# Performance work log

Measured on AMD Instinct MI355X. Metric: run time of the kernel, lower is better.

## Reference

```python
import jax, jax.numpy as jnp
import numpy as np

N_NODES = 50000
N_EDGES = 1600000
IN_FEATS = 512
N_HIDDEN = 128
N_CLASSES = 40


def setup_inputs() -> dict:
    key = jax.random.key(0)
    k1, k2, k3, k4, k5, k6, k7 = jax.random.split(key, 7)
    features = jax.random.normal(k1, (N_NODES, IN_FEATS), dtype=jnp.float32)
    src = jax.random.randint(k2, (N_EDGES,), 0, N_NODES)
    dst = jax.random.randint(k3, (N_EDGES,), 0, N_NODES)
    # Glorot-ish init for weights, zeros for biases (DGL GraphConv defaults)
    W1 = jax.random.normal(k4, (IN_FEATS, N_HIDDEN), dtype=jnp.float32) / np.sqrt(IN_FEATS)
    b1 = jnp.zeros((N_HIDDEN,), dtype=jnp.float32)
    W2 = jax.random.normal(k5, (N_HIDDEN, N_CLASSES), dtype=jnp.float32) / np.sqrt(N_HIDDEN)
    b2 = jnp.zeros((N_CLASSES,), dtype=jnp.float32)
    return {"features": features, "W1": W1, "b1": b1, "W2": W2, "b2": b2,
            "src": src, "dst": dst}


def _norms(src, dst, n_nodes):
    ones = jnp.ones(src.shape[0], dtype=jnp.float32)
    deg_out = jax.ops.segment_sum(ones, src, num_segments=n_nodes)
    deg_in = jax.ops.segment_sum(ones, dst, num_segments=n_nodes)
    # clamp degree >= 1 as DGL does
    norm_src = jax.lax.rsqrt(jnp.maximum(deg_out, 1.0))
    norm_dst = jax.lax.rsqrt(jnp.maximum(deg_in, 1.0))
    return norm_src, norm_dst


def _graph_conv(x, W, b, src, dst, norm_src, norm_dst, n_nodes):
    # DGL GraphConv with norm='both'; in_feats > out_feats so W applied first
    h = x @ W                                   # [N, out]
    h = h * norm_src[:, None]                   # src-side D^{-1/2}
    msgs = h[src]                               # gather [E, out]
    agg = jax.ops.segment_sum(msgs, dst, num_segments=n_nodes)  # scatter-add
    agg = agg * norm_dst[:, None]               # dst-side D^{-1/2}
    return agg + b


def reference(features, W1, b1, W2, b2, src, dst):
    norm_src, norm_dst = _norms(src, dst, N_NODES)
    h = _graph_conv(features, W1, b1, src, dst, norm_src, norm_dst, N_NODES)
    h = jax.nn.relu(h)
    # dropout is identity at inference
    h = _graph_conv(h, W2, b2, src, dst, norm_src, norm_dst, N_NODES)
    return h
```

## Files before the change

kernel.cpp:

```cpp
#include <hip/hip_runtime.h>
#include <hip/hip_bf16.h>

#define N_NODES 50000
#define N_EDGES 1600000
#define IN_FEATS 512
#define N_HIDDEN 128
#define N_CLASSES 40
#define NBKT 782
#define NBLK 800
#define EPB 2000
#define NROWPAD 50048

typedef __attribute__((ext_vector_type(8))) short bf16x8;
typedef __attribute__((ext_vector_type(4))) float f32x4;

__device__ __forceinline__ unsigned short f2bf(float f) {
    unsigned u = __float_as_uint(f);
    u = (u + 0x7FFFu + ((u >> 16) & 1u)) >> 16;
    return (unsigned short)u;
}
__device__ __forceinline__ float bf2f(unsigned short h) {
    return __uint_as_float(((unsigned)h) << 16);
}
__device__ __forceinline__ unsigned pk_bf(float a, float b) {
    __hip_bfloat162 h = __float22bfloat162_rn(make_float2(a, b));
    union { __hip_bfloat162 v; unsigned u; } c;
    c.v = h;
    return c.u;
}

__device__ __forceinline__ void cvt8(float4 a, float4 b, bf16x8& h, bf16x8& l) {
    unsigned h0 = pk_bf(a.x, a.y), h1 = pk_bf(a.z, a.w);
    unsigned h2 = pk_bf(b.x, b.y), h3 = pk_bf(b.z, b.w);
    unsigned l0 = pk_bf(a.x - __uint_as_float(h0 << 16),
                        a.y - __uint_as_float(h0 & 0xffff0000u));
    unsigned l1 = pk_bf(a.z - __uint_as_float(h1 << 16),
                        a.w - __uint_as_float(h1 & 0xffff0000u));
    unsigned l2 = pk_bf(b.x - __uint_as_float(h2 << 16),
                        b.y - __uint_as_float(h2 & 0xffff0000u));
    unsigned l3 = pk_bf(b.z - __uint_as_float(h3 << 16),
                        b.w - __uint_as_float(h3 & 0xffff0000u));
    union U { unsigned u[4]; bf16x8 v; };
    U H; H.u[0] = h0; H.u[1] = h1; H.u[2] = h2; H.u[3] = h3; h = H.v;
    U L; L.u[0] = l0; L.u[1] = l1; L.u[2] = l2; L.u[3] = l3; l = L.v;
}

__device__ __forceinline__ int imin(int a, int b) { return a < b ? a : b; }

__global__ __launch_bounds__(256) void setup_cvt(
    const float* __restrict__ W1, const float* __restrict__ W2,
    unsigned short* __restrict__ W1ch, unsigned short* __restrict__ W1cl,
    unsigned short* __restrict__ W2th, unsigned short* __restrict__ W2tl) {
    int i = blockIdx.x * 256 + threadIdx.x;
    if (i < IN_FEATS * N_HIDDEN) {
        int k = i >> 7, c = i & 127;
        float v = W1[i];
        unsigned short h = f2bf(v);
        int o = (k >> 5) * 4096 + c * 32 + (k & 31);
        W1ch[o] = h;
        W1cl[o] = f2bf(v - bf2f(h));
    } else {
        int j = i - IN_FEATS * N_HIDDEN;
        int n = j >> 7, k = j & 127;
        float v = (n < N_CLASSES) ? W2[k * N_CLASSES + n] : 0.f;
        unsigned short h = f2bf(v);
        W2th[n * 128 + k] = h;
        W2tl[n * 128 + k] = f2bf(v - bf2f(h));
    }
}


#define MFJ(AH, AL, BH, BL, ACC)                                              \
    ACC = __builtin_amdgcn_mfma_f32_16x16x32_bf16(AH, BH, ACC, 0, 0, 0);      \
    ACC = __builtin_amdgcn_mfma_f32_16x16x32_bf16(AH, BL, ACC, 0, 0, 0);      \
    ACC = __builtin_amdgcn_mfma_f32_16x16x32_bf16(AL, BH, ACC, 0, 0, 0);

#define CHUNK_COMPUTE(FRAGBASE, KC)                                           \
    {                                                                         \
        const unsigned short* wk  = wbh + (KC) * 4096;                        \
        const unsigned short* wkl = wbl + (KC) * 4096;                        \
        bf16x8 bh0 = *(const bf16x8*)(wk);                                    \
        bf16x8 bh1 = *(const bf16x8*)(wk + 512);                              \
        bf16x8 bl0 = *(const bf16x8*)(wkl);                                   \
        bf16x8 bl1 = *(const bf16x8*)(wkl + 512);                             \
        const unsigned short* fb = (FRAGBASE);                                \
        bf16x8 ah0 = *(const bf16x8*)(fb + (0 * 64 + lane) * 8);              \
        bf16x8 ah1 = *(const bf16x8*)(fb + (1 * 64 + lane) * 8);              \
        bf16x8 ah2 = *(const bf16x8*)(fb + (2 * 64 + lane) * 8);              \
        bf16x8 ah3 = *(const bf16x8*)(fb + (3 * 64 + lane) * 8);              \
        bf16x8 al0 = *(const bf16x8*)(fb + 2048 + (0 * 64 + lane) * 8);       \
        bf16x8 al1 = *(const bf16x8*)(fb + 2048 + (1 * 64 + lane) * 8);       \
        bf16x8 al2 = *(const bf16x8*)(fb + 2048 + (2 * 64 + lane) * 8);       \
        bf16x8 al3 = *(const bf16x8*)(fb + 2048 + (3 * 64 + lane) * 8);       \
        MFJ(ah0, al0, bh0, bl0, acc[0][0]) MFJ(ah0, al0, bh1, bl1, acc[0][1]) \
        MFJ(ah1, al1, bh0, bl0, acc[1][0]) MFJ(ah1, al1, bh1, bl1, acc[1][1]) \
        MFJ(ah2, al2, bh0, bl0, acc[2][0]) MFJ(ah2, al2, bh1, bl1, acc[2][1]) \
        MFJ(ah3, al3, bh0, bl0, acc[3][0]) MFJ(ah3, al3, bh1, bl1, acc[3][1]) \
    }

__global__ __launch_bounds__(256) void megaA(
    const int* __restrict__ src, const int* __restrict__ dst,
    int* __restrict__ histD, int* __restrict__ histS,
    const float* __restrict__ X, const unsigned short* __restrict__ Wch,
    const unsigned short* __restrict__ Wcl, unsigned short* __restrict__ Hb) {
    __shared__ __align__(16) unsigned char smem[32768];
    const int tid = threadIdx.x;

    if (blockIdx.x >= NBKT) {
        int* hd = (int*)smem;
        int* hs = hd + NBKT;
        int b = blockIdx.x - NBKT;
        for (int i = tid; i < NBKT; i += 256) { hd[i] = 0; hs[i] = 0; }
        __syncthreads();
        int e0 = b * EPB;
        for (int i = tid; i < EPB; i += 256) {
            atomicAdd(&hd[dst[e0 + i] >> 6], 1);
            atomicAdd(&hs[src[e0 + i] >> 6], 1);
        }
        __syncthreads();
        for (int i = tid; i < NBKT; i += 256) {
            histD[b * NBKT + i] = hd[i];
            histS[b * NBKT + i] = hs[i];
        }
        return;
    }
    typedef unsigned short ush;
    ush* lds = (ush*)smem;

    const int lane = tid & 63;
    const int wv = tid >> 6;
    const int m = lane & 15;
    const int q = lane >> 4;
    const int q8 = q * 8;
    const int row0 = blockIdx.x * 64;

    const unsigned short* wbh = Wch + (wv * 32 + m) * 32 + q8;
    const unsigned short* wbl = Wcl + (wv * 32 + m) * 32 + q8;

    const int srow = (tid >> 6) * 16 + (tid & 15);
    const int sq8  = ((tid >> 4) & 3) * 8;
    const float* xp = &X[(size_t)imin(row0 + srow, N_NODES - 1) * IN_FEATS + sq8];

    f32x4 acc[4][2];
#pragma unroll
    for (int i = 0; i < 4; i++)
#pragma unroll
        for (int j = 0; j < 2; j++) acc[i][j] = (f32x4){0.f, 0.f, 0.f, 0.f};

    {
        float4 c00 = *(const float4*)(xp),      c01 = *(const float4*)(xp + 4);
        float4 c10 = *(const float4*)(xp + 32), c11 = *(const float4*)(xp + 36);
        bf16x8 h, l;
        cvt8(c00, c01, h, l);
        *(bf16x8*)(lds + tid * 8) = h;
        *(bf16x8*)(lds + 2048 + tid * 8) = l;
        cvt8(c10, c11, h, l);
        *(bf16x8*)(lds + 4096 + tid * 8) = h;
        *(bf16x8*)(lds + 6144 + tid * 8) = l;
    }
    float4 a00 = *(const float4*)(xp + 64), a01 = *(const float4*)(xp + 68);
    float4 a10 = *(const float4*)(xp + 96), a11 = *(const float4*)(xp + 100);
    __syncthreads();

    for (int pp = 0; pp < 8; pp++) {
        if (pp < 7) {
            ush* bs = lds + ((pp + 1) & 1) * 8192;
            bf16x8 h, l;
            cvt8(a00, a01, h, l);
            *(bf16x8*)(bs + tid * 8) = h;
            *(bf16x8*)(bs + 2048 + tid * 8) = l;
            cvt8(a10, a11, h, l);
            *(bf16x8*)(bs + 4096 + tid * 8) = h;
            *(bf16x8*)(bs + 6144 + tid * 8) = l;
        }
        if (pp < 6) {
            const float* xq = xp + (pp + 2) * 64;
            a00 = *(const float4*)(xq);      a01 = *(const float4*)(xq + 4);
            a10 = *(const float4*)(xq + 32); a11 = *(const float4*)(xq + 36);
        }
        const ush* br = lds + (pp & 1) * 8192;
        CHUNK_COMPUTE(br,        2 * pp)
        CHUNK_COMPUTE(br + 4096, 2 * pp + 1)
        if (pp < 7) __syncthreads();
    }

#pragma unroll
    for (int i = 0; i < 4; i++) {
#pragma unroll
        for (int r = 0; r < 4; r++) {
            int grow = row0 + i * 16 + q * 4 + r;
            if (grow < N_NODES) {
#pragma unroll
                for (int j = 0; j < 2; j++)
                    Hb[(size_t)grow * N_HIDDEN + wv * 32 + j * 16 + m] = f2bf(acc[i][j][r]);
            }
        }
    }
}

__global__ __launch_bounds__(256) void p2_local(
    const int* __restrict__ histD, const int* __restrict__ histS,
    int* __restrict__ baseD, int* __restrict__ baseS,
    int* __restrict__ totD, int* __restrict__ totS) {
    int wv = threadIdx.x >> 6, lane = threadIdx.x & 63;
    int w = blockIdx.x * 4 + wv;
    if (w >= NBKT) return;
    int runD = 0, runS = 0;
#pragma unroll
    for (int c = 0; c < 13; c++) {
        int blk = c * 64 + lane;
        int vD = 0, vS = 0;
        if (blk < NBLK) {
            vD = histD[blk * NBKT + w];
            vS = histS[blk * NBKT + w];
        }
        int iD = vD, iS = vS;
#pragma unroll
        for (int off = 1; off < 64; off <<= 1) {
            int tD = __shfl_up(iD, off);
            int tS = __shfl_up(iS, off);
            if (lane >= off) { iD += tD; iS += tS; }
        }
        if (blk < NBLK) {
            baseD[blk * NBKT + w] = runD + iD - vD;
            baseS[blk * NBKT + w] = runS + iS - vS;
        }
        runD += __shfl(iD, 63);
        runS += __shfl(iS, 63);
    }
    if (lane == 0) { totD[w] = runD; totS[w] = runS; }
}

__global__ __launch_bounds__(1024) void p2_small(
    const int* __restrict__ totD, const int* __restrict__ totS,
    int* __restrict__ bucket_base, int* __restrict__ srcb_base,
    int* __restrict__ offsets) {
    __shared__ int part[1024];
    int t = threadIdx.x;
    int v = (t < NBKT) ? totD[t] : 0;
    part[t] = v;
    __syncthreads();
    for (int off = 1; off < 1024; off <<= 1) {
        int x = (t >= off) ? part[t - off] : 0;
        __syncthreads();
        part[t] += x;
        __syncthreads();
    }
    if (t < NBKT) bucket_base[t] = part[t] - v;
    if (t == 0) { bucket_base[NBKT] = N_EDGES; offsets[N_NODES] = N_EDGES; }
    __syncthreads();
    v = (t < NBKT) ? totS[t] : 0;
    part[t] = v;
    __syncthreads();
    for (int off = 1; off < 1024; off <<= 1) {
        int x = (t >= off) ? part[t - off] : 0;
        __syncthreads();
        part[t] += x;
        __syncthreads();
    }
    if (t < NBKT) srcb_base[t] = part[t] - v;
    if (t == 0) srcb_base[NBKT] = N_EDGES;
}

__global__ __launch_bounds__(256) void p3_scatter(
    const int* __restrict__ src, const int* __restrict__ dst,
    const int* __restrict__ baseD, const int* __restrict__ baseS,
    const int* __restrict__ bucket_base, const int* __restrict__ srcb_base,
    unsigned int* __restrict__ edata, unsigned char* __restrict__ srcv) {
    __shared__ int curD[NBKT], curS[NBKT];
    int t = threadIdx.x, b = blockIdx.x;
    for (int i = t; i < NBKT; i += 256) {
        curD[i] = bucket_base[i] + baseD[b * NBKT + i];
        curS[i] = srcb_base[i] + baseS[b * NBKT + i];
    }
    __syncthreads();
    int e0 = b * EPB;
    for (int i = t; i < EPB; i += 256) {
        int s = src[e0 + i], d = dst[e0 + i];
        int slotD = atomicAdd(&curD[d >> 6], 1);
        edata[slotD] = (unsigned)s | ((unsigned)(d & 63) << 16);
        int slotS = atomicAdd(&curS[s >> 6], 1);
        srcv[slotS] = (unsigned char)(s & 63);
    }
}

__global__ __launch_bounds__(256) void p4_fused(
    const int* __restrict__ srcb_base, const unsigned char* __restrict__ srcv,
    const int* __restrict__ bucket_base, const unsigned int* __restrict__ edata,
    int* __restrict__ offsets, float* __restrict__ norm_src,
    float* __restrict__ norm_dst, unsigned short* __restrict__ sorted_src) {
    __shared__ int cntS[64], cntD[64], cur[64];
    int t = threadIdx.x, b = blockIdx.x;
    if (t < 64) { cntS[t] = 0; cntD[t] = 0; }
    __syncthreads();
    int s0 = srcb_base[b], s1 = srcb_base[b + 1];
    for (int i = s0 + t; i < s1; i += 256) atomicAdd(&cntS[srcv[i]], 1);
    int d0 = bucket_base[b], d1 = bucket_base[b + 1];
    for (int i = d0 + t; i < d1; i += 256)
        atomicAdd(&cntD[(edata[i] >> 16) & 63], 1);
    __syncthreads();
    if (t == 0) {
        int run = 0;
        for (int i = 0; i < 64; i++) { cur[i] = run; run += cntD[i]; }
    }
    __syncthreads();
    if (t < 64) {
        int node = b * 64 + t;
        if (node < N_NODES) {
            norm_src[node] = rsqrtf(fmaxf((float)cntS[t], 1.0f));
            offsets[node] = d0 + cur[t];
            norm_dst[node] = rsqrtf(fmaxf((float)cntD[t], 1.0f));
        }
    }
    __syncthreads();
    for (int i = d0 + t; i < d1; i += 256) {
        unsigned e = edata[i];
        int slot = atomicAdd(&cur[(e >> 16) & 63], 1);
        sorted_src[d0 + slot] = (unsigned short)(e & 0xFFFFu);
    }
}

#define FMA8(W, NS)                                                   \
    acc0 = fmaf(__uint_as_float((W).x << 16), NS, acc0);              \
    acc1 = fmaf(__uint_as_float((W).x & 0xffff0000u), NS, acc1);      \
    acc2 = fmaf(__uint_as_float((W).y << 16), NS, acc2);              \
    acc3 = fmaf(__uint_as_float((W).y & 0xffff0000u), NS, acc3);      \
    acc4 = fmaf(__uint_as_float((W).z << 16), NS, acc4);              \
    acc5 = fmaf(__uint_as_float((W).z & 0xffff0000u), NS, acc5);      \
    acc6 = fmaf(__uint_as_float((W).w << 16), NS, acc6);              \
    acc7 = fmaf(__uint_as_float((W).w & 0xffff0000u), NS, acc7);

__global__ __launch_bounds__(256) void agg1_kernel(
    const int* __restrict__ offsets, const unsigned short* __restrict__ sorted_src,
    const unsigned short* __restrict__ Hb, const float* __restrict__ norm_dst,
    const float* __restrict__ norm_src, const float* __restrict__ b1,
    unsigned short* __restrict__ H1h, unsigned short* __restrict__ H1l) {
    int wid = (blockIdx.x * 256 + threadIdx.x) >> 6;
    int lane = threadIdx.x & 63;
    if (wid >= N_NODES) return;
    int start = offsets[wid], end = offsets[wid + 1];
    int quad = lane >> 4;
    int c8 = (lane & 15) * 8;
    float acc0 = 0.f, acc1 = 0.f, acc2 = 0.f, acc3 = 0.f;
    float acc4 = 0.f, acc5 = 0.f, acc6 = 0.f, acc7 = 0.f;
    int base = start;
    for (; base + 16 <= end; base += 16) {
        int e0 = sorted_src[base + quad];
        int e1 = sorted_src[base + 4 + quad];
        int e2 = sorted_src[base + 8 + quad];
        int e3 = sorted_src[base + 12 + quad];
        float n0 = norm_src[e0], n1 = norm_src[e1];
        float n2 = norm_src[e2], n3 = norm_src[e3];
        uint4 w0 = *(const uint4*)&Hb[(size_t)e0 * N_HIDDEN + c8];
        uint4 w1 = *(const uint4*)&Hb[(size_t)e1 * N_HIDDEN + c8];
        uint4 w2 = *(const uint4*)&Hb[(size_t)e2 * N_HIDDEN + c8];
        uint4 w3 = *(const uint4*)&Hb[(size_t)e3 * N_HIDDEN + c8];
        FMA8(w0, n0);
        FMA8(w1, n1);
        FMA8(w2, n2);
        FMA8(w3, n3);
    }
    for (; base + 4 <= end; base += 4) {
        int e = sorted_src[base + quad];
        float n = norm_src[e];
        uint4 w = *(const uint4*)&Hb[(size_t)e * N_HIDDEN + c8];
        FMA8(w, n);
    }
    int rem = end - base;
    if (quad < rem) {
        int e = sorted_src[base + quad];
        float n = norm_src[e];
        uint4 w = *(const uint4*)&Hb[(size_t)e * N_HIDDEN + c8];
        FMA8(w, n);
    }
    acc0 += __shfl_xor(acc0, 16); acc0 += __shfl_xor(acc0, 32);
    acc1 += __shfl_xor(acc1, 16); acc1 += __shfl_xor(acc1, 32);
    acc2 += __shfl_xor(acc2, 16); acc2 += __shfl_xor(acc2, 32);
    acc3 += __shfl_xor(acc3, 16); acc3 += __shfl_xor(acc3, 32);
    acc4 += __shfl_xor(acc4, 16); acc4 += __shfl_xor(acc4, 32);
    acc5 += __shfl_xor(acc5, 16); acc5 += __shfl_xor(acc5, 32);
    acc6 += __shfl_xor(acc6, 16); acc6 += __shfl_xor(acc6, 32);
    acc7 += __shfl_xor(acc7, 16); acc7 += __shfl_xor(acc7, 32);
    if (quad == 0) {
        float nd = norm_dst[wid];
        float ns = norm_src[wid];
        float4 ba = *(const float4*)&b1[c8];
        float4 bb = *(const float4*)&b1[c8 + 4];
        float o[8];
        o[0] = fmaxf(acc0 * nd + ba.x, 0.f) * ns;
        o[1] = fmaxf(acc1 * nd + ba.y, 0.f) * ns;
        o[2] = fmaxf(acc2 * nd + ba.z, 0.f) * ns;
        o[3] = fmaxf(acc3 * nd + ba.w, 0.f) * ns;
        o[4] = fmaxf(acc4 * nd + bb.x, 0.f) * ns;
        o[5] = fmaxf(acc5 * nd + bb.y, 0.f) * ns;
        o[6] = fmaxf(acc6 * nd + bb.z, 0.f) * ns;
        o[7] = fmaxf(acc7 * nd + bb.w, 0.f) * ns;
        unsigned short hh[8], ll[8];
#pragma unroll
        for (int t = 0; t < 8; t++) {
            hh[t] = f2bf(o[t]);
            ll[t] = f2bf(o[t] - bf2f(hh[t]));
        }
        uint4 ph = make_uint4((unsigned)hh[0] | ((unsigned)hh[1] << 16),
                              (unsigned)hh[2] | ((unsigned)hh[3] << 16),
                              (unsigned)hh[4] | ((unsigned)hh[5] << 16),
                              (unsigned)hh[6] | ((unsigned)hh[7] << 16));
        uint4 pl = make_uint4((unsigned)ll[0] | ((unsigned)ll[1] << 16),
                              (unsigned)ll[2] | ((unsigned)ll[3] << 16),
                              (unsigned)ll[4] | ((unsigned)ll[5] << 16),
                              (unsigned)ll[6] | ((unsigned)ll[7] << 16));
        *(uint4*)&H1h[(size_t)wid * N_HIDDEN + c8] = ph;
        *(uint4*)&H1l[(size_t)wid * N_HIDDEN + c8] = pl;
    }
}

__global__ __launch_bounds__(256) void gemm2_kernel(
    const unsigned short* __restrict__ H1h, const unsigned short* __restrict__ H1l,
    const unsigned short* __restrict__ W2th, const unsigned short* __restrict__ W2tl,
    unsigned int* __restrict__ H2u) {
    __shared__ __align__(16) unsigned short Bh[48][136];
    __shared__ __align__(16) unsigned short Bl[48][136];
    const int tid = threadIdx.x;
    for (int i = tid; i < 48 * 16; i += 256) {
        int n = i >> 4, kq = (i & 15) * 8;
        *(uint4*)&Bh[n][kq] = *(const uint4*)&W2th[n * 128 + kq];
        *(uint4*)&Bl[n][kq] = *(const uint4*)&W2tl[n * 128 + kq];
    }
    __syncthreads();
    const int lane = tid & 63;
    const int wave = tid >> 6;
    const int m = lane & 15;
    const int q = lane >> 4;
    const int row0 = blockIdx.x * 128 + wave * 32;

    f32x4 acc[2][3];
#pragma unroll
    for (int i = 0; i < 2; i++)
#pragma unroll
        for (int j = 0; j < 3; j++) acc[i][j] = (f32x4){0.f, 0.f, 0.f, 0.f};

#pragma unroll
    for (int kc = 0; kc < 4; kc++) {
        bf16x8 bh[3], bl[3];
#pragma unroll
        for (int j = 0; j < 3; j++) {
            bh[j] = *(const bf16x8*)&Bh[j * 16 + m][kc * 32 + q * 8];
            bl[j] = *(const bf16x8*)&Bl[j * 16 + m][kc * 32 + q * 8];
        }
#pragma unroll
        for (int i = 0; i < 2; i++) {
            size_t ro = (size_t)(row0 + i * 16 + m) * N_HIDDEN + kc * 32 + q * 8;
            bf16x8 ah = *(const bf16x8*)&H1h[ro];
            bf16x8 al = *(const bf16x8*)&H1l[ro];
#pragma unroll
            for (int j = 0; j < 3; j++) {
                acc[i][j] = __builtin_amdgcn_mfma_f32_16x16x32_bf16(ah, bh[j], acc[i][j], 0, 0, 0);
                acc[i][j] = __builtin_amdgcn_mfma_f32_16x16x32_bf16(ah, bl[j], acc[i][j], 0, 0, 0);
                acc[i][j] = __builtin_amdgcn_mfma_f32_16x16x32_bf16(al, bh[j], acc[i][j], 0, 0, 0);
            }
        }
    }
#pragma unroll
    for (int i = 0; i < 2; i++) {
#pragma unroll
        for (int r = 0; r < 4; r++) {
            int row = row0 + i * 16 + q * 4 + r;
            if (row < N_NODES) {
#pragma unroll
                for (int j = 0; j < 3; j++) {
                    int col = j * 16 + m;
                    if (col < N_CLASSES) {
                        float v = acc[i][j][r];
                        unsigned short h = f2bf(v);
                        unsigned short l = f2bf(v - bf2f(h));
                        H2u[(size_t)row * 48 + col] = ((unsigned)h << 16) | (unsigned)l;
                    }
                }
            }
        }
    }
}

#define ACC4(V)                                                               \
    acc.x += __uint_as_float((V).x & 0xffff0000u) + __uint_as_float((V).x << 16); \
    acc.y += __uint_as_float((V).y & 0xffff0000u) + __uint_as_float((V).y << 16); \
    acc.z += __uint_as_float((V).z & 0xffff0000u) + __uint_as_float((V).z << 16); \
    acc.w += __uint_as_float((V).w & 0xffff0000u) + __uint_as_float((V).w << 16);

__global__ __launch_bounds__(256) void agg2_kernel(
    const int* __restrict__ offsets, const unsigned short* __restrict__ sorted_src,
    const unsigned int* __restrict__ H2u, const float* __restrict__ norm_dst,
    const float* __restrict__ b2, float* __restrict__ OUT) {
    int wid = (blockIdx.x * 256 + threadIdx.x) >> 6;
    int lane = threadIdx.x & 63;
    if (wid >= N_NODES) return;
    int start = offsets[wid], end = offsets[wid + 1];
    int quad = lane >> 4;
    int c4 = (lane & 15) * 4;
    bool active = c4 < N_CLASSES;
    float4 acc = make_float4(0.f, 0.f, 0.f, 0.f);
    int base = start;
    for (; base + 16 <= end; base += 16) {
        int e0 = sorted_src[base + quad];
        int e1 = sorted_src[base + 4 + quad];
        int e2 = sorted_src[base + 8 + quad];
        int e3 = sorted_src[base + 12 + quad];
        if (active) {
            uint4 v0 = *(const uint4*)&H2u[(size_t)e0 * 48 + c4];
            uint4 v1 = *(const uint4*)&H2u[(size_t)e1 * 48 + c4];
            uint4 v2 = *(const uint4*)&H2u[(size_t)e2 * 48 + c4];
            uint4 v3 = *(const uint4*)&H2u[(size_t)e3 * 48 + c4];
            ACC4(v0); ACC4(v1); ACC4(v2); ACC4(v3);
        }
    }
    for (; base + 4 <= end; base += 4) {
        int e = sorted_src[base + quad];
        if (active) {
            uint4 v = *(const uint4*)&H2u[(size_t)e * 48 + c4];
            ACC4(v);
        }
    }
    int rem = end - base;
    if (quad < rem && active) {
        int e = sorted_src[base + quad];
        uint4 v = *(const uint4*)&H2u[(size_t)e * 48 + c4];
        ACC4(v);
    }
    acc.x += __shfl_xor(acc.x, 16); acc.x += __shfl_xor(acc.x, 32);
    acc.y += __shfl_xor(acc.y, 16); acc.y += __shfl_xor(acc.y, 32);
    acc.z += __shfl_xor(acc.z, 16); acc.z += __shfl_xor(acc.z, 32);
    acc.w += __shfl_xor(acc.w, 16); acc.w += __shfl_xor(acc.w, 32);
    if (lane < 10) {
        float nd = norm_dst[wid];
        float4 b = *(const float4*)&b2[lane * 4];
        acc.x = acc.x * nd + b.x;
        acc.y = acc.y * nd + b.y;
        acc.z = acc.z * nd + b.z;
        acc.w = acc.w * nd + b.w;
        *(float4*)&OUT[(size_t)wid * N_CLASSES + lane * 4] = acc;
    }
}

extern "C" void kernel_launch(void* const* d_in, const int* in_sizes, int n_in,
                              void* d_out, int out_size, void* d_ws, size_t ws_size,
                              hipStream_t stream) {
    const float* X   = (const float*)d_in[0];
    const float* W1  = (const float*)d_in[1];
    const float* b1  = (const float*)d_in[2];
    const float* W2  = (const float*)d_in[3];
    const float* b2  = (const float*)d_in[4];
    const int*   src = (const int*)d_in[5];
    const int*   dst = (const int*)d_in[6];
    float* out = (float*)d_out;

    float* norm_src   = (float*)d_ws;
    float* norm_dst   = norm_src + N_NODES;
    int*   offsets    = (int*)(norm_dst + N_NODES);
    int*   bucket_base = offsets + N_NODES + 16;
    int*   srcb_base  = bucket_base + 800;
    unsigned int* edata = (unsigned int*)(srcb_base + 800);
    unsigned char* srcv = (unsigned char*)(edata + N_EDGES);
    unsigned short* sorted_src =
        (unsigned short*)((int*)(edata + N_EDGES) + 400000);
    int*   regionA    = (int*)(edata + N_EDGES) + 400000 + 800000;
    int*   histD      = regionA;
    int*   histS      = regionA + 625600;
    int*   baseD      = regionA + 1251200;
    int*   baseS      = regionA + 1876800;
    int*   totD       = regionA + 2502400;
    int*   totS       = regionA + 2503200;
    unsigned int* H2u = (unsigned int*)regionA;
    unsigned short* H1h = (unsigned short*)(regionA + 3200000);
    unsigned short* H1l = H1h + (size_t)NROWPAD * N_HIDDEN;
    unsigned short* W1ch = H1l + (size_t)NROWPAD * N_HIDDEN;
    unsigned short* W1cl = W1ch + IN_FEATS * N_HIDDEN;
    unsigned short* W2th = W1cl + IN_FEATS * N_HIDDEN;
    unsigned short* W2tl = W2th + 48 * 128;
    unsigned short* Hb   = W2tl + 48 * 128;

    setup_cvt<<<(IN_FEATS * N_HIDDEN + 48 * 128) / 256, 256, 0, stream>>>(
        W1, W2, W1ch, W1cl, W2th, W2tl);
    megaA<<<NBLK + NBKT, 256, 0, stream>>>(src, dst, histD, histS, X, W1ch, W1cl, Hb);
    p2_local<<<(NBKT + 3) / 4, 256, 0, stream>>>(histD, histS, baseD, baseS, totD, totS);
    p2_small<<<1, 1024, 0, stream>>>(totD, totS, bucket_base, srcb_base, offsets);
    p3_scatter<<<NBLK, 256, 0, stream>>>(src, dst, baseD, baseS, bucket_base, srcb_base,
                                         edata, srcv);
    p4_fused<<<NBKT, 256, 0, stream>>>(srcb_base, srcv, bucket_base, edata,
                                       offsets, norm_src, norm_dst, sorted_src);
    agg1_kernel<<<(N_NODES + 3) / 4, 256, 0, stream>>>(offsets, sorted_src, Hb, norm_dst,
                                                       norm_src, b1, H1h, H1l);
    gemm2_kernel<<<(N_NODES + 127) / 128, 256, 0, stream>>>(H1h, H1l, W2th, W2tl, H2u);
    agg2_kernel<<<(N_NODES + 3) / 4, 256, 0, stream>>>(offsets, sorted_src, H2u, norm_dst, b2, out);
}
```

Baseline: 357.1 us.

## Fuse second-layer GEMM into agg1 epilogue and drop H1 intermediate

The standalone MFMA gemm2 kernel is removed. agg1 now multiplies each node's ReLU'd hidden vector by a transposed fp32 W2 directly, using per-lane FMAs and a 16-lane shuffle reduction, then writes the split-bf16 H2 row. This avoids writing and re-reading the hi/lo bf16 H1 buffers and saves one kernel launch. H2 row padding shrinks from 48 to 40 words, which also trims the agg2 gather footprint. In exchange every agg1 wave does extra shuffle reductions and W2 loads in its epilogue.

Measured after the change: 384.9 us. 1.08x slower.

```diff
diff --git a/kernel.cpp b/kernel.cpp
--- a/kernel.cpp
+++ b/kernel.cpp
@@ -9,7 +9,6 @@
 #define NBKT 782
 #define NBLK 800
 #define EPB 2000
-#define NROWPAD 50048
 
 typedef __attribute__((ext_vector_type(8))) short bf16x8;
 typedef __attribute__((ext_vector_type(4))) float f32x4;
@@ -50,7 +49,7 @@
 __global__ __launch_bounds__(256) void setup_cvt(
     const float* __restrict__ W1, const float* __restrict__ W2,
     unsigned short* __restrict__ W1ch, unsigned short* __restrict__ W1cl,
-    unsigned short* __restrict__ W2th, unsigned short* __restrict__ W2tl) {
+    float* __restrict__ W2tf) {
     int i = blockIdx.x * 256 + threadIdx.x;
     if (i < IN_FEATS * N_HIDDEN) {
         int k = i >> 7, c = i & 127;
@@ -61,11 +60,8 @@
         W1cl[o] = f2bf(v - bf2f(h));
     } else {
         int j = i - IN_FEATS * N_HIDDEN;
-        int n = j >> 7, k = j & 127;
-        float v = (n < N_CLASSES) ? W2[k * N_CLASSES + n] : 0.f;
-        unsigned short h = f2bf(v);
-        W2th[n * 128 + k] = h;
-        W2tl[n * 128 + k] = f2bf(v - bf2f(h));
+        int c = j >> 7, k = j & 127;
+        W2tf[j] = W2[k * N_CLASSES + c];
     }
 }
 
@@ -334,13 +330,14 @@
     const int* __restrict__ offsets, const unsigned short* __restrict__ sorted_src,
     const unsigned short* __restrict__ Hb, const float* __restrict__ norm_dst,
     const float* __restrict__ norm_src, const float* __restrict__ b1,
-    unsigned short* __restrict__ H1h, unsigned short* __restrict__ H1l) {
+    const float* __restrict__ W2tf, unsigned int* __restrict__ H2u) {
     int wid = (blockIdx.x * 256 + threadIdx.x) >> 6;
     int lane = threadIdx.x & 63;
     if (wid >= N_NODES) return;
     int start = offsets[wid], end = offsets[wid + 1];
     int quad = lane >> 4;
-    int c8 = (lane & 15) * 8;
+    int m = lane & 15;
+    int c8 = m * 8;
     float acc0 = 0.f, acc1 = 0.f, acc2 = 0.f, acc3 = 0.f;
     float acc4 = 0.f, acc5 = 0.f, acc6 = 0.f, acc7 = 0.f;
     int base = start;
@@ -381,102 +378,48 @@
     acc5 += __shfl_xor(acc5, 16); acc5 += __shfl_xor(acc5, 32);
     acc6 += __shfl_xor(acc6, 16); acc6 += __shfl_xor(acc6, 32);
     acc7 += __shfl_xor(acc7, 16); acc7 += __shfl_xor(acc7, 32);
-    if (quad == 0) {
-        float nd = norm_dst[wid];
-        float ns = norm_src[wid];
-        float4 ba = *(const float4*)&b1[c8];
-        float4 bb = *(const float4*)&b1[c8 + 4];
-        float o[8];
-        o[0] = fmaxf(acc0 * nd + ba.x, 0.f) * ns;
-        o[1] = fmaxf(acc1 * nd + ba.y, 0.f) * ns;
-        o[2] = fmaxf(acc2 * nd + ba.z, 0.f) * ns;
-        o[3] = fmaxf(acc3 * nd + ba.w, 0.f) * ns;
-        o[4] = fmaxf(acc4 * nd + bb.x, 0.f) * ns;
-        o[5] = fmaxf(acc5 * nd + bb.y, 0.f) * ns;
-        o[6] = fmaxf(acc6 * nd + bb.z, 0.f) * ns;
-        o[7] = fmaxf(acc7 * nd + bb.w, 0.f) * ns;
-        unsigned short hh[8], ll[8];
-#pragma unroll
-        for (int t = 0; t < 8; t++) {
-            hh[t] = f2bf(o[t]);
-            ll[t] = f2bf(o[t] - bf2f(hh[t]));
-        }
-        uint4 ph = make_uint4((unsigned)hh[0] | ((unsigned)hh[1] << 16),
-                              (unsigned)hh[2] | ((unsigned)hh[3] << 16),
-                              (unsigned)hh[4] | ((unsigned)hh[5] << 16),
-                              (unsigned)hh[6] | ((unsigned)hh[7] << 16));
-        uint4 pl = make_uint4((unsigned)ll[0] | ((unsigned)ll[1] << 16),
-                              (unsigned)ll[2] | ((unsigned)ll[3] << 16),
-                              (unsigned)ll[4] | ((unsigned)ll[5] << 16),
-                              (unsigned)ll[6] | ((unsigned)ll[7] << 16));
-        *(uint4*)&H1h[(size_t)wid * N_HIDDEN + c8] = ph;
-        *(uint4*)&H1l[(size_t)wid * N_HIDDEN + c8] = pl;
-    }
-}
-
-__global__ __launch_bounds__(256) void gemm2_kernel(
-    const unsigned short* __restrict__ H1h, const unsigned short* __restrict__ H1l,
-    const unsigned short* __restrict__ W2th, const unsigned short* __restrict__ W2tl,
-    unsigned int* __restrict__ H2u) {
-    __shared__ __align__(16) unsigned short Bh[48][136];
-    __shared__ __align__(16) unsigned short Bl[48][136];
-    const int tid = threadIdx.x;
-    for (int i = tid; i < 48 * 16; i += 256) {
-        int n = i >> 4, kq = (i & 15) * 8;
-        *(uint4*)&Bh[n][kq] = *(const uint4*)&W2th[n * 128 + kq];
-        *(uint4*)&Bl[n][kq] = *(const uint4*)&W2tl[n * 128 + kq];
-    }
-    __syncthreads();
-    const int lane = tid & 63;
-    const int wave = tid >> 6;
-    const int m = lane & 15;
-    const int q = lane >> 4;
-    const int row0 = blockIdx.x * 128 + wave * 32;
-
-    f32x4 acc[2][3];
-#pragma unroll
-    for (int i = 0; i < 2; i++)
-#pragma unroll
-        for (int j = 0; j < 3; j++) acc[i][j] = (f32x4){0.f, 0.f, 0.f, 0.f};
-
-#pragma unroll
-    for (int kc = 0; kc < 4; kc++) {
-        bf16x8 bh[3], bl[3];
-#pragma unroll
-        for (int j = 0; j < 3; j++) {
-            bh[j] = *(const bf16x8*)&Bh[j * 16 + m][kc * 32 + q * 8];
-            bl[j] = *(const bf16x8*)&Bl[j * 16 + m][kc * 32 + q * 8];
-        }
-#pragma unroll
-        for (int i = 0; i < 2; i++) {
-            size_t ro = (size_t)(row0 + i * 16 + m) * N_HIDDEN + kc * 32 + q * 8;
-            bf16x8 ah = *(const bf16x8*)&H1h[ro];
-            bf16x8 al = *(const bf16x8*)&H1l[ro];
-#pragma unroll
-            for (int j = 0; j < 3; j++) {
-                acc[i][j] = __builtin_amdgcn_mfma_f32_16x16x32_bf16(ah, bh[j], acc[i][j], 0, 0, 0);
-                acc[i][j] = __builtin_amdgcn_mfma_f32_16x16x32_bf16(ah, bl[j], acc[i][j], 0, 0, 0);
-                acc[i][j] = __builtin_amdgcn_mfma_f32_16x16x32_bf16(al, bh[j], acc[i][j], 0, 0, 0);
-            }
-        }
-    }
-#pragma unroll
-    for (int i = 0; i < 2; i++) {
-#pragma unroll
-        for (int r = 0; r < 4; r++) {
-            int row = row0 + i * 16 + q * 4 + r;
-            if (row < N_NODES) {
-#pragma unroll
-                for (int j = 0; j < 3; j++) {
-                    int col = j * 16 + m;
-                    if (col < N_CLASSES) {
-                        float v = acc[i][j][r];
-                        unsigned short h = f2bf(v);
-                        unsigned short l = f2bf(v - bf2f(h));
-                        H2u[(size_t)row * 48 + col] = ((unsigned)h << 16) | (unsigned)l;
-                    }
-                }
-            }
+
+    float nd = norm_dst[wid];
+    float ns = norm_src[wid];
+    float4 ba = *(const float4*)&b1[c8];
+    float4 bb = *(const float4*)&b1[c8 + 4];
+    float h0 = fmaxf(acc0 * nd + ba.x, 0.f) * ns;
+    float h1 = fmaxf(acc1 * nd + ba.y, 0.f) * ns;
+    float h2 = fmaxf(acc2 * nd + ba.z, 0.f) * ns;
+    float h3 = fmaxf(acc3 * nd + ba.w, 0.f) * ns;
+    float h4 = fmaxf(acc4 * nd + bb.x, 0.f) * ns;
+    float h5 = fmaxf(acc5 * nd + bb.y, 0.f) * ns;
+    float h6 = fmaxf(acc6 * nd + bb.z, 0.f) * ns;
+    float h7 = fmaxf(acc7 * nd + bb.w, 0.f) * ns;
+
+    float pc[10];
+#pragma unroll
+    for (int c = 0; c < 10; c++) {
+        const float* wr = W2tf + (quad * 10 + c) * 128 + c8;
+        float4 wa = *(const float4*)wr;
+        float4 wb2 = *(const float4*)(wr + 4);
+        float s = fmaf(h0, wa.x, 0.f);
+        s = fmaf(h1, wa.y, s);
+        s = fmaf(h2, wa.z, s);
+        s = fmaf(h3, wa.w, s);
+        s = fmaf(h4, wb2.x, s);
+        s = fmaf(h5, wb2.y, s);
+        s = fmaf(h6, wb2.z, s);
+        s = fmaf(h7, wb2.w, s);
+        pc[c] = s;
+    }
+#pragma unroll
+    for (int off = 1; off < 16; off <<= 1) {
+#pragma unroll
+        for (int c = 0; c < 10; c++) pc[c] += __shfl_xor(pc[c], off);
+    }
+    if (m == 0) {
+#pragma unroll
+        for (int c = 0; c < 10; c++) {
+            float v = pc[c];
+            unsigned short hh = f2bf(v);
+            unsigned short ll = f2bf(v - bf2f(hh));
+            H2u[(size_t)wid * 40 + quad * 10 + c] = ((unsigned)hh << 16) | (unsigned)ll;
         }
     }
 }
@@ -506,24 +449,24 @@
         int e2 = sorted_src[base + 8 + quad];
         int e3 = sorted_src[base + 12 + quad];
         if (active) {
-            uint4 v0 = *(const uint4*)&H2u[(size_t)e0 * 48 + c4];
-            uint4 v1 = *(const uint4*)&H2u[(size_t)e1 * 48 + c4];
-            uint4 v2 = *(const uint4*)&H2u[(size_t)e2 * 48 + c4];
-            uint4 v3 = *(const uint4*)&H2u[(size_t)e3 * 48 + c4];
+            uint4 v0 = *(const uint4*)&H2u[(size_t)e0 * 40 + c4];
+            uint4 v1 = *(const uint4*)&H2u[(size_t)e1 * 40 + c4];
+            uint4 v2 = *(const uint4*)&H2u[(size_t)e2 * 40 + c4];
+            uint4 v3 = *(const uint4*)&H2u[(size_t)e3 * 40 + c4];
             ACC4(v0); ACC4(v1); ACC4(v2); ACC4(v3);
         }
     }
     for (; base + 4 <= end; base += 4) {
         int e = sorted_src[base + quad];
         if (active) {
-            uint4 v = *(const uint4*)&H2u[(size_t)e * 48 + c4];
+            uint4 v = *(const uint4*)&H2u[(size_t)e * 40 + c4];
             ACC4(v);
         }
     }
     int rem = end - base;
     if (quad < rem && active) {
         int e = sorted_src[base + quad];
-        uint4 v = *(const uint4*)&H2u[(size_t)e * 48 + c4];
+        uint4 v = *(const uint4*)&H2u[(size_t)e * 40 + c4];
         ACC4(v);
     }
     acc.x += __shfl_xor(acc.x, 16); acc.x += __shfl_xor(acc.x, 32);
@@ -570,16 +513,13 @@
     int*   totD       = regionA + 2502400;
     int*   totS       = regionA + 2503200;
     unsigned int* H2u = (unsigned int*)regionA;
-    unsigned short* H1h = (unsigned short*)(regionA + 3200000);
-    unsigned short* H1l = H1h + (size_t)NROWPAD * N_HIDDEN;
-    unsigned short* W1ch = H1l + (size_t)NROWPAD * N_HIDDEN;
+    unsigned short* W1ch = (unsigned short*)(regionA + 3200000);
     unsigned short* W1cl = W1ch + IN_FEATS * N_HIDDEN;
-    unsigned short* W2th = W1cl + IN_FEATS * N_HIDDEN;
-    unsigned short* W2tl = W2th + 48 * 128;
-    unsigned short* Hb   = W2tl + 48 * 128;
-
-    setup_cvt<<<(IN_FEATS * N_HIDDEN + 48 * 128) / 256, 256, 0, stream>>>(
-        W1, W2, W1ch, W1cl, W2th, W2tl);
+    float* W2tf          = (float*)(W1cl + IN_FEATS * N_HIDDEN);
+    unsigned short* Hb   = (unsigned short*)(W2tf + N_CLASSES * N_HIDDEN);
+
+    setup_cvt<<<(IN_FEATS * N_HIDDEN + N_CLASSES * N_HIDDEN) / 256, 256, 0, stream>>>(
+        W1, W2, W1ch, W1cl, W2tf);
     megaA<<<NBLK + NBKT, 256, 0, stream>>>(src, dst, histD, histS, X, W1ch, W1cl, Hb);
     p2_local<<<(NBKT + 3) / 4, 256, 0, stream>>>(histD, histS, baseD, baseS, totD, totS);
     p2_small<<<1, 1024, 0, stream>>>(totD, totS, bucket_base, srcb_base, offsets);
@@ -588,7 +528,6 @@
     p4_fused<<<NBKT, 256, 0, stream>>>(srcb_base, srcv, bucket_base, edata,
                                        offsets, norm_src, norm_dst, sorted_src);
     agg1_kernel<<<(N_NODES + 3) / 4, 256, 0, stream>>>(offsets, sorted_src, Hb, norm_dst,
-                                                       norm_src, b1, H1h, H1l);
-    gemm2_kernel<<<(N_NODES + 127) / 128, 256, 0, stream>>>(H1h, H1l, W2th, W2tl, H2u);
+                                                       norm_src, b1, W2tf, H2u);
     agg2_kernel<<<(N_NODES + 3) / 4, 256, 0, stream>>>(offsets, sorted_src, H2u, norm_dst, b2, out);
 }
```
